# Kernel tuning notes

Measured on AMD Instinct MI355X. Metric: run time of the kernel, lower is better.

The kernel has to match this reference:

```python
import jax, jax.numpy as jnp
import numpy as np

C = 1.0                 # Poincare ball curvature
PROJ_EPS = 1e-5         # boundary epsilon for projection
ACOSH_EPS = 1e-7        # numerical floor for arccosh argument


def setup_inputs() -> dict:
    key = jax.random.key(0)
    k1, k2 = jax.random.split(key)
    num_tokens, embed_dim = 30522, 64
    batch, seq = 4, 1024
    token_ids = jax.random.randint(k1, (batch, seq), 0, num_tokens, dtype=jnp.int64)
    weight = jax.random.normal(k2, (num_tokens, embed_dim), dtype=jnp.float32) * 0.05
    scale = jnp.asarray(0.5, dtype=jnp.float32)
    return {"token_ids": token_ids, "weight": weight, "scale": scale}


def _poincare_bias(token_ids, weight, scale):
    ids = jnp.clip(token_ids, 0, weight.shape[0] - 1)
    emb = weight[ids]                                   # (b, s, d)
    # project onto the Poincare ball: clip norm to (1 - eps) / sqrt(c)
    sqc = jnp.sqrt(C)
    max_norm = (1.0 - PROJ_EPS) / sqc
    norm = jnp.linalg.norm(emb, axis=-1, keepdims=True)
    emb = jnp.where(norm > max_norm, emb * (max_norm / jnp.maximum(norm, 1e-12)), emb)
    # pairwise hyperbolic distance via arccosh form (== Mobius-add/artanh form):
    # d(x,y) = (1/sqrt(c)) * arccosh(1 + 2c||x-y||^2 / ((1-c||x||^2)(1-c||y||^2)))
    x2 = jnp.sum(emb * emb, axis=-1)                    # (b, s)
    gram = jnp.einsum("bid,bjd->bij", emb, emb)        # (b, s, s)
    sqdist = jnp.maximum(x2[:, :, None] + x2[:, None, :] - 2.0 * gram, 0.0)
    denom = (1.0 - C * x2)[:, :, None] * (1.0 - C * x2)[:, None, :]
    arg = 1.0 + 2.0 * C * sqdist / denom
    dist = jnp.arccosh(jnp.maximum(arg, 1.0 + ACOSH_EPS)) / sqc
    return scale * -dist                                # (b, s, s)


def reference(token_ids, weight, scale):
    return _poincare_bias(token_ids, weight, scale)
```

## Files before the change

kernel.cpp:

```cpp
#include <hip/hip_runtime.h>
#include <hip/hip_bf16.h>

typedef __attribute__((ext_vector_type(8)))  short bf16x8;
typedef __attribute__((ext_vector_type(4)))  float f32x4;
typedef __attribute__((ext_vector_type(16))) float f32x16;

#define EMB_DIM 64

__global__ __launch_bounds__(256) void gather_project_kernel(
    const int* __restrict__ ids, const float* __restrict__ weight,
    __hip_bfloat16* __restrict__ emb, float* __restrict__ x2,
    int n_tokens_total, int vocab)
{
    int token = blockIdx.x * 4 + (threadIdx.x >> 6);
    int lane  = threadIdx.x & 63;
    if (token >= n_tokens_total) return;

    int id = ids[token];
    id = min(max(id, 0), vocab - 1);

    float w = weight[(size_t)id * EMB_DIM + lane];

    float s = w * w;
    #pragma unroll
    for (int off = 32; off >= 1; off >>= 1) s += __shfl_xor(s, off);
    float nrm = sqrtf(s);
    const float max_norm = 0.99999f;
    if (nrm > max_norm) w *= max_norm / fmaxf(nrm, 1e-12f);

    __hip_bfloat16 h = __float2bfloat16(w);
    float hf = __bfloat162float(h);
    emb[(size_t)token * EMB_DIM + lane] = h;

    float s2 = hf * hf;
    #pragma unroll
    for (int off = 32; off >= 1; off >>= 1) s2 += __shfl_xor(s2, off);
    if (lane == 0) x2[token] = s2;
}

__global__ __launch_bounds__(256) void pair_bias_kernel(
    const __hip_bfloat16* __restrict__ emb, const float* __restrict__ x2,
    const float* __restrict__ scale_p, float* __restrict__ out, int S)
{
    const int b    = blockIdx.z;
    const int wid  = threadIdx.x >> 6;
    const int lane = threadIdx.x & 63;
    const int i0   = blockIdx.y * 64 + (wid >> 1) * 32;
    const int j0   = blockIdx.x * 64 + (wid & 1) * 32;
    const int m    = lane & 31;
    const int h    = lane >> 5;

    const short* E  = (const short*)emb + (size_t)b * S * EMB_DIM;
    const short* Ea = E + (i0 + m) * EMB_DIM + h * 8;
    const short* Eb = E + (j0 + m) * EMB_DIM + h * 8;

    f32x16 acc = {};
    #pragma unroll
    for (int kb = 0; kb < 4; ++kb) {
        bf16x8 av = *(const bf16x8*)(Ea + kb * 16);
        bf16x8 bv = *(const bf16x8*)(Eb + kb * 16);
        acc = __builtin_amdgcn_mfma_f32_32x32x16_bf16(av, bv, acc, 0, 0, 0);
    }

    const float* x2B = x2 + (size_t)b * S;
    const float  xj    = x2B[j0 + m];
    const float  scale = scale_p[0];
    const float  omxj  = 1.f - xj;

    float* O = out + ((size_t)b * S + i0 + 4 * h) * S + j0 + m;

    #pragma unroll
    for (int g = 0; g < 4; ++g) {
        f32x4 xi4 = *(const f32x4*)(x2B + i0 + g * 8 + 4 * h);
        #pragma unroll
        for (int e = 0; e < 4; ++e) {
            float gv = acc[g * 4 + e];
            float xi = xi4[e];
            float sq  = fmaxf(xi + xj - 2.f * gv, 0.f);
            float den = (1.f - xi) * omxj;
            float u = fmaxf(2.f * sq * __builtin_amdgcn_rcpf(den), 1.1920929e-7f);
            float w = 1.f + u + __builtin_amdgcn_sqrtf(u * (u + 2.f));
            float dist = 0.69314718056f * __builtin_amdgcn_logf(w);
            O[(size_t)(g * 8 + e) * S] = -scale * dist;
        }
    }
}

extern "C" void kernel_launch(void* const* d_in, const int* in_sizes, int n_in,
                              void* d_out, int out_size, void* d_ws, size_t ws_size,
                              hipStream_t stream) {
    const int*   ids     = (const int*)d_in[0];
    const float* weight  = (const float*)d_in[1];
    const float* scale_p = (const float*)d_in[2];
    float*       out     = (float*)d_out;

    const int n_tok = in_sizes[0];
    const int vocab = in_sizes[1] / EMB_DIM;
    const int S     = out_size / n_tok;
    const int B     = n_tok / S;

    __hip_bfloat16* emb = (__hip_bfloat16*)d_ws;
    float* x2 = (float*)((char*)d_ws + (size_t)n_tok * EMB_DIM * sizeof(__hip_bfloat16));

    gather_project_kernel<<<(n_tok + 3) / 4, 256, 0, stream>>>(
        ids, weight, emb, x2, n_tok, vocab);

    dim3 grid(S / 64, S / 64, B);
    pair_bias_kernel<<<grid, 256, 0, stream>>>(emb, x2, scale_p, out, S);
}
```

Before: 74.30 us.

## Fuse gather/projection into pair-bias kernel using LDS-staged embedding tiles

Removes the separate gather/project kernel and its workspace round trip. Each 64x64 output tile block gathers its 128 token rows from the weight table, projects them and converts to bf16 into padded LDS, then runs the MFMA gram and distance epilogue from LDS. This drops one kernel launch and the global emb/x2 writes and reads. In exchange, every block redoes the gather and projection for its rows, about 16x redundant weight reads per token across the grid, which should mostly hit cache.

Measured after the change: 72.76 us (median of 2 runs). 2.1% less time.

```diff
diff --git a/kernel.cpp b/kernel.cpp
--- a/kernel.cpp
+++ b/kernel.cpp
@@ -6,72 +6,90 @@
 typedef __attribute__((ext_vector_type(16))) float f32x16;
 
 #define EMB_DIM 64
+#define LDS_STRIDE 72
 
-__global__ __launch_bounds__(256) void gather_project_kernel(
+__global__ __launch_bounds__(256) void fused_bias_kernel(
     const int* __restrict__ ids, const float* __restrict__ weight,
-    __hip_bfloat16* __restrict__ emb, float* __restrict__ x2,
-    int n_tokens_total, int vocab)
+    const float* __restrict__ scale_p, float* __restrict__ out,
+    int S, int vocab)
 {
-    int token = blockIdx.x * 4 + (threadIdx.x >> 6);
-    int lane  = threadIdx.x & 63;
-    if (token >= n_tokens_total) return;
+    __shared__ short Es[128 * LDS_STRIDE];
+    __shared__ float x2s[128];
 
-    int id = ids[token];
-    id = min(max(id, 0), vocab - 1);
+    const int b  = blockIdx.z;
+    const int i0 = blockIdx.y * 64;
+    const int j0 = blockIdx.x * 64;
+    const int t  = threadIdx.x;
 
-    float w = weight[(size_t)id * EMB_DIM + lane];
+    {
+        const int r  = t >> 1;
+        const int h2 = t & 1;
+        const int grow = (r < 64) ? (i0 + r) : (j0 + r - 64);
+        int id = ids[(size_t)b * S + grow];
+        id = min(max(id, 0), vocab - 1);
 
-    float s = w * w;
-    #pragma unroll
-    for (int off = 32; off >= 1; off >>= 1) s += __shfl_xor(s, off);
-    float nrm = sqrtf(s);
-    const float max_norm = 0.99999f;
-    if (nrm > max_norm) w *= max_norm / fmaxf(nrm, 1e-12f);
+        const f32x4* W = (const f32x4*)(weight + (size_t)id * EMB_DIM + h2 * 32);
+        f32x4 v[8];
+        #pragma unroll
+        for (int k = 0; k < 8; ++k) v[k] = W[k];
 
-    __hip_bfloat16 h = __float2bfloat16(w);
-    float hf = __bfloat162float(h);
-    emb[(size_t)token * EMB_DIM + lane] = h;
+        float s = 0.f;
+        #pragma unroll
+        for (int k = 0; k < 8; ++k)
+            s += v[k].x * v[k].x + v[k].y * v[k].y + v[k].z * v[k].z + v[k].w * v[k].w;
+        s += __shfl_xor(s, 1);
 
-    float s2 = hf * hf;
-    #pragma unroll
-    for (int off = 32; off >= 1; off >>= 1) s2 += __shfl_xor(s2, off);
-    if (lane == 0) x2[token] = s2;
-}
+        const float max_norm = 0.99999f;
+        float nrm = sqrtf(s);
+        float mul = (nrm > max_norm) ? (max_norm / fmaxf(nrm, 1e-12f)) : 1.f;
 
-__global__ __launch_bounds__(256) void pair_bias_kernel(
-    const __hip_bfloat16* __restrict__ emb, const float* __restrict__ x2,
-    const float* __restrict__ scale_p, float* __restrict__ out, int S)
-{
-    const int b    = blockIdx.z;
-    const int wid  = threadIdx.x >> 6;
-    const int lane = threadIdx.x & 63;
-    const int i0   = blockIdx.y * 64 + (wid >> 1) * 32;
-    const int j0   = blockIdx.x * 64 + (wid & 1) * 32;
-    const int m    = lane & 31;
-    const int h    = lane >> 5;
+        const float* vf = (const float*)v;
+        bf16x8 hv[4];
+        float s2 = 0.f;
+        #pragma unroll
+        for (int k = 0; k < 32; ++k) {
+            __hip_bfloat16 hb = __float2bfloat16(vf[k] * mul);
+            float hf = __bfloat162float(hb);
+            s2 += hf * hf;
+            hv[k >> 3][k & 7] = __builtin_bit_cast(short, hb);
+        }
+        s2 += __shfl_xor(s2, 1);
 
-    const short* E  = (const short*)emb + (size_t)b * S * EMB_DIM;
-    const short* Ea = E + (i0 + m) * EMB_DIM + h * 8;
-    const short* Eb = E + (j0 + m) * EMB_DIM + h * 8;
+        short* dst = Es + r * LDS_STRIDE + h2 * 32;
+        #pragma unroll
+        for (int k = 0; k < 4; ++k)
+            *(bf16x8*)(dst + k * 8) = hv[k];
+        if (h2 == 0) x2s[r] = s2;
+    }
+    __syncthreads();
+
+    const int wid  = t >> 6;
+    const int lane = t & 63;
+    const int m  = lane & 31;
+    const int h  = lane >> 5;
+    const int ia = (wid >> 1) * 32;
+    const int jb = (wid & 1) * 32;
+
+    const short* Ear = Es + (ia + m) * LDS_STRIDE + h * 8;
+    const short* Ebr = Es + (64 + jb + m) * LDS_STRIDE + h * 8;
 
     f32x16 acc = {};
     #pragma unroll
     for (int kb = 0; kb < 4; ++kb) {
-        bf16x8 av = *(const bf16x8*)(Ea + kb * 16);
-        bf16x8 bv = *(const bf16x8*)(Eb + kb * 16);
+        bf16x8 av = *(const bf16x8*)(Ear + kb * 16);
+        bf16x8 bv = *(const bf16x8*)(Ebr + kb * 16);
         acc = __builtin_amdgcn_mfma_f32_32x32x16_bf16(av, bv, acc, 0, 0, 0);
     }
 
-    const float* x2B = x2 + (size_t)b * S;
-    const float  xj    = x2B[j0 + m];
-    const float  scale = scale_p[0];
-    const float  omxj  = 1.f - xj;
+    const float xj    = x2s[64 + jb + m];
+    const float scale = scale_p[0];
+    const float omxj  = 1.f - xj;
 
-    float* O = out + ((size_t)b * S + i0 + 4 * h) * S + j0 + m;
+    float* O = out + ((size_t)b * S + i0 + ia + 4 * h) * S + j0 + jb + m;
 
     #pragma unroll
     for (int g = 0; g < 4; ++g) {
-        f32x4 xi4 = *(const f32x4*)(x2B + i0 + g * 8 + 4 * h);
+        f32x4 xi4 = *(const f32x4*)(x2s + ia + g * 8 + 4 * h);
         #pragma unroll
         for (int e = 0; e < 4; ++e) {
             float gv = acc[g * 4 + e];
@@ -99,12 +117,6 @@
     const int S     = out_size / n_tok;
     const int B     = n_tok / S;
 
-    __hip_bfloat16* emb = (__hip_bfloat16*)d_ws;
-    float* x2 = (float*)((char*)d_ws + (size_t)n_tok * EMB_DIM * sizeof(__hip_bfloat16));
-
-    gather_project_kernel<<<(n_tok + 3) / 4, 256, 0, stream>>>(
-        ids, weight, emb, x2, n_tok, vocab);
-
     dim3 grid(S / 64, S / 64, B);
-    pair_bias_kernel<<<grid, 256, 0, stream>>>(emb, x2, scale_p, out, S);
+    fused_bias_kernel<<<grid, 256, 0, stream>>>(ids, weight, scale_p, out, S, vocab);
 }
```
